# Optimization experiments

Measured on AMD Instinct MI355X. Metric: run time of the kernel, lower is better.

## Reference

```python
import jax, jax.numpy as jnp
import numpy as np

C = 256
H = 8
D = C // H


def setup_inputs() -> dict:
    key = jax.random.key(0)
    ks = jax.random.split(key, 6)
    scale = 1.0 / np.sqrt(C)
    x = jax.random.normal(ks[0], (8, C, 2048), dtype=jnp.float32)
    Wq = jax.random.normal(ks[1], (C, C), dtype=jnp.float32) * scale
    Wk = jax.random.normal(ks[2], (C, C), dtype=jnp.float32) * scale
    Wv = jax.random.normal(ks[3], (C, C), dtype=jnp.float32) * scale
    Wo = jax.random.normal(ks[4], (C, C), dtype=jnp.float32) * scale
    bo = jax.random.normal(ks[5], (C,), dtype=jnp.float32) * 0.01
    return {"x": x, "Wq": Wq, "Wk": Wk, "Wv": Wv, "Wo": Wo, "bo": bo}


def reference(x, Wq, Wk, Wv, Wo, bo):
    # x: [N, C, L]; Conv1d(k=1) == per-position matmul with weight [out, in]
    q = jnp.einsum('oc,ncl->nol', Wq, x)
    k = jnp.einsum('oc,ncl->nol', Wk, x)
    v = jnp.einsum('oc,ncl->nol', Wv, x)
    N, _, L = x.shape
    # rearrange 'n (h d) l -> n l h d'
    q = q.reshape(N, H, D, L).transpose(0, 3, 1, 2)
    k = k.reshape(N, H, D, L).transpose(0, 3, 1, 2)
    v = v.reshape(N, H, D, L).transpose(0, 3, 1, 2)
    qk = jnp.einsum('nqhd,nkhd->nhqk', q, k)
    # NOTE: original scales by full embedding size (channels), not head_dim
    attn = jax.nn.softmax(qk * (C ** -0.5), axis=3)
    out = jnp.einsum('nhql,nlhd->nqhd', attn, v)
    # rearrange 'n l h d -> n (h d) l'
    out = out.transpose(0, 2, 3, 1).reshape(N, C, L)
    return jnp.einsum('oc,ncl->nol', Wo, out) + bo[None, :, None]
```

## Files before the change

kernel.cpp:

```cpp
#include <hip/hip_runtime.h>


typedef __bf16 bf8 __attribute__((ext_vector_type(8)));
typedef float f4 __attribute__((ext_vector_type(4)));
typedef float f32x4 __attribute__((ext_vector_type(4)));
typedef unsigned short u16;
typedef unsigned int u32;
typedef u16 u16x4 __attribute__((ext_vector_type(4)));
typedef u16 u16x8 __attribute__((ext_vector_type(8)));

__device__ __forceinline__ u16 f2bf(float f) {
  __bf16 h = (__bf16)f;
  return __builtin_bit_cast(u16, h);
}
__device__ __forceinline__ float bf2f(u16 b) {
  union { u32 u; float f; } v; v.u = ((u32)b) << 16;
  return v.f;
}
__device__ __forceinline__ u32 pk2bf(float a, float b) {
  return ((u32)f2bf(b) << 16) | (u32)f2bf(a);
}
__device__ __forceinline__ u32 pktrunc(float a, float b) {
  return __builtin_amdgcn_perm(__builtin_bit_cast(u32, b),
                               __builtin_bit_cast(u32, a), 0x07060302u);
}
__device__ __forceinline__ float exp2_fast(float x) {
  return __builtin_amdgcn_exp2f(x);
}

#define MFMA(a, b, c) __builtin_amdgcn_mfma_f32_16x16x32_bf16((a), (b), (c), 0, 0, 0)

union bf8u { u32 u[4]; bf8 v; };
__device__ __forceinline__ bf8 mkbf8(u32 a, u32 b, u32 c, u32 d) {
  bf8u t; t.u[0] = a; t.u[1] = b; t.u[2] = c; t.u[3] = d; return t.v;
}

__global__ __launch_bounds__(256) void convert_weights(
    const float* __restrict__ Wq, const float* __restrict__ Wk,
    const float* __restrict__ Wv, const float* __restrict__ Wo,
    const float* __restrict__ bo,
    u16* __restrict__ Wqb, u16* __restrict__ Wkb, u16* __restrict__ Wvb,
    u16* __restrict__ Wob, u16* __restrict__ bob) {
  const int tid = threadIdx.x;
  const int seg = blockIdx.x >> 6;
  const int blk = blockIdx.x & 63;
  const float* s; u16* d;
  if (seg == 0)      { s = Wq; d = Wqb; }
  else if (seg == 1) { s = Wk; d = Wkb; }
  else if (seg == 2) { s = Wv; d = Wvb; }
  else               { s = Wo; d = Wob; }
  const int base = blk * 1024 + tid * 4;
  f32x4 v = *(const f32x4*)(s + base);
  u16x4 o;
#pragma unroll
  for (int i = 0; i < 4; ++i) o[i] = f2bf(v[i]);
  *(u16x4*)(d + base) = o;
  if (blockIdx.x == 0 && tid < 64) {
    const int bb = tid * 4;
    f32x4 bv = *(const f32x4*)(bo + bb);
    u16x4 ob;
#pragma unroll
    for (int i = 0; i < 4; ++i) ob[i] = f2bf(bv[i]);
    *(u16x4*)(bob + bb) = ob;
  }
}

__global__ __launch_bounds__(256) void qkv_proj(
    const float* __restrict__ x, const u16* __restrict__ Wq,
    const u16* __restrict__ Wk, const u16* __restrict__ Wv,
    u16* __restrict__ qbuf, u16* __restrict__ kbuf, u16* __restrict__ vbuf) {
  __shared__ __align__(16) u16 xt[2][64 * 40];
  const int n = blockIdx.z;
  const int o0 = blockIdx.y * 64;
  const int l0 = blockIdx.x * 64;
  const int tid = threadIdx.x;
  const int w = tid >> 6, lane = tid & 63, quad = lane >> 4, l16 = lane & 15;
  const int ow = o0 + w * 16;
  const float SC = 0.09019327066650391f;

  f4 acc[3][4];
#pragma unroll
  for (int p = 0; p < 3; ++p)
#pragma unroll
    for (int lt = 0; lt < 4; ++lt) acc[p][lt] = (f4){0.f, 0.f, 0.f, 0.f};

  const int cp = tid >> 4;
  const int lq = (tid & 15) * 4;

  auto stage = [&](int c0, int buf) {
    const float* xp = x + (n * 256 + c0 + 2 * cp) * 2048 + l0 + lq;
    f32x4 r0 = *(const f32x4*)xp;
    f32x4 r1 = *(const f32x4*)(xp + 2048);
#pragma unroll
    for (int i = 0; i < 4; ++i)
      *(u32*)&xt[buf][(lq + i) * 40 + 2 * cp] = pk2bf(r0[i], r1[i]);
  };

  stage(0, 0);
  for (int s = 0; s < 8; ++s) {
    __syncthreads();
    if (s < 7) stage((s + 1) * 32, (s + 1) & 1);
    const int c0 = s * 32;
    bf8 a0 = *(const bf8*)(Wq + (ow + l16) * 256 + c0 + quad * 8);
    bf8 a1 = *(const bf8*)(Wk + (ow + l16) * 256 + c0 + quad * 8);
    bf8 a2 = *(const bf8*)(Wv + (ow + l16) * 256 + c0 + quad * 8);
    const u16* xb = xt[s & 1];
#pragma unroll
    for (int lt = 0; lt < 4; ++lt) {
      bf8 b = *(const bf8*)&xb[(lt * 16 + l16) * 40 + quad * 8];
      acc[0][lt] = MFMA(a0, b, acc[0][lt]);
      acc[1][lt] = MFMA(a1, b, acc[1][lt]);
      acc[2][lt] = MFMA(a2, b, acc[2][lt]);
    }
  }
  const int hh = ow >> 5;
  const int dbase = (ow & 31) + quad * 4;
#pragma unroll
  for (int lt = 0; lt < 4; ++lt) {
    const int l = l0 + lt * 16 + l16;
    const int vpos = l0 + (lt >> 1) * 32 + (l16 >> 2) * 8 + (l16 & 3) + (lt & 1) * 4;
    const size_t base = ((size_t)(n * 8 + hh) * 2048 + l) * 32 + dbase;
    u16x4 qv, kv;
#pragma unroll
    for (int r = 0; r < 4; ++r) {
      qv[r] = f2bf(acc[0][lt][r] * SC);
      kv[r] = f2bf(acc[1][lt][r]);
    }
    *(u16x4*)(qbuf + base) = qv;
    *(u16x4*)(kbuf + base) = kv;
#pragma unroll
    for (int r = 0; r < 4; ++r)
      vbuf[(n * 256 + ow + quad * 4 + r) * 2048 + vpos] = f2bf(acc[2][lt][r]);
  }
}

__global__ __launch_bounds__(256) void attn(
    const u16* __restrict__ qbuf, const u16* __restrict__ kbuf,
    const u16* __restrict__ vbuf, u16* __restrict__ abuf) {
  __shared__ float Osh[3][64][37];
  const int head = blockIdx.x, qblk = blockIdx.y;
  const int n = head >> 3, h = head & 7;
  const int tid = threadIdx.x;
  const int w = tid >> 6, lane = tid & 63;
  const int quad = lane >> 4, l16 = lane & 15;
  const int q0 = qblk * 64;
  const int kc0 = w * 512;

  const u16* kb = kbuf + (size_t)head * 2048 * 32 + l16 * 32 + quad * 8;
  const u16* vb = vbuf + ((size_t)n * 256 + h * 32 + l16) * 2048 + quad * 8;

  const bf8 ones = mkbf8(0x3F803F80u, 0x3F803F80u, 0x3F803F80u, 0x3F803F80u);

  bf8 aq[4];
#pragma unroll
  for (int qt = 0; qt < 4; ++qt)
    aq[qt] = *(const bf8*)(qbuf + ((size_t)head * 2048 + q0 + qt * 16 + l16) * 32 + quad * 8);

  f4 O[2][4];
  f4 Lacc[4];
#pragma unroll
  for (int qt = 0; qt < 4; ++qt) {
    O[0][qt] = (f4){0.f, 0.f, 0.f, 0.f};
    O[1][qt] = (f4){0.f, 0.f, 0.f, 0.f};
    Lacc[qt] = (f4){0.f, 0.f, 0.f, 0.f};
  }

  bf8 bk[4], vf[4];
#pragma unroll
  for (int kt = 0; kt < 4; ++kt) bk[kt] = *(const bf8*)(kb + (kc0 + kt * 16) * 32);
#pragma unroll
  for (int dt = 0; dt < 2; ++dt)
#pragma unroll
    for (int g = 0; g < 2; ++g)
      vf[dt * 2 + g] = *(const bf8*)(vb + dt * 16 * 2048 + kc0 + g * 32);

  for (int kc = kc0; kc < kc0 + 512; kc += 64) {
    const int kn = (kc < kc0 + 448) ? kc + 64 : kc0;
    bf8 nk[4], nv[4];
#pragma unroll
    for (int kt = 0; kt < 4; ++kt) nk[kt] = *(const bf8*)(kb + (kn + kt * 16) * 32);
#pragma unroll
    for (int dt = 0; dt < 2; ++dt)
#pragma unroll
      for (int g = 0; g < 2; ++g)
        nv[dt * 2 + g] = *(const bf8*)(vb + dt * 16 * 2048 + kn + g * 32);

#pragma unroll
    for (int qt = 0; qt < 4; ++qt) {
      f4 z = (f4){0.f, 0.f, 0.f, 0.f};
      f4 s0 = MFMA(bk[0], aq[qt], z);
      f4 s1 = MFMA(bk[1], aq[qt], z);
      f4 s2 = MFMA(bk[2], aq[qt], z);
      f4 s3 = MFMA(bk[3], aq[qt], z);
      f4 e0, e1, e2, e3;
#pragma unroll
      for (int r = 0; r < 4; ++r) {
        e0[r] = exp2_fast(s0[r]);
        e1[r] = exp2_fast(s1[r]);
        e2[r] = exp2_fast(s2[r]);
        e3[r] = exp2_fast(s3[r]);
      }
      bf8 B0 = mkbf8(pktrunc(e0[0], e0[1]), pktrunc(e0[2], e0[3]),
                     pktrunc(e1[0], e1[1]), pktrunc(e1[2], e1[3]));
      bf8 B1 = mkbf8(pktrunc(e2[0], e2[1]), pktrunc(e2[2], e2[3]),
                     pktrunc(e3[0], e3[1]), pktrunc(e3[2], e3[3]));
      Lacc[qt] = MFMA(ones, B0, Lacc[qt]);
      Lacc[qt] = MFMA(ones, B1, Lacc[qt]);
#pragma unroll
      for (int dt = 0; dt < 2; ++dt) {
        f4 o = O[dt][qt];
        o = MFMA(vf[dt * 2 + 0], B0, o);
        o = MFMA(vf[dt * 2 + 1], B1, o);
        O[dt][qt] = o;
      }
    }
#pragma unroll
    for (int i = 0; i < 4; ++i) { bk[i] = nk[i]; vf[i] = nv[i]; }
  }

  if (w > 0) {
#pragma unroll
    for (int dt = 0; dt < 2; ++dt)
#pragma unroll
      for (int qt = 0; qt < 4; ++qt)
#pragma unroll
        for (int r = 0; r < 4; ++r)
          Osh[w - 1][lane][dt * 16 + qt * 4 + r] = O[dt][qt][r];
#pragma unroll
    for (int qt = 0; qt < 4; ++qt)
      Osh[w - 1][lane][32 + qt] = Lacc[qt][0];
  }
  __syncthreads();
  if (w == 0) {
#pragma unroll
    for (int p = 0; p < 3; ++p) {
#pragma unroll
      for (int dt = 0; dt < 2; ++dt)
#pragma unroll
        for (int qt = 0; qt < 4; ++qt)
#pragma unroll
          for (int r = 0; r < 4; ++r)
            O[dt][qt][r] += Osh[p][lane][dt * 16 + qt * 4 + r];
#pragma unroll
      for (int qt = 0; qt < 4; ++qt)
        Lacc[qt][0] += Osh[p][lane][32 + qt];
    }
#pragma unroll
    for (int qt = 0; qt < 4; ++qt) {
      const float inv = 1.0f / Lacc[qt][0];
      const int q = q0 + qt * 16 + l16;
#pragma unroll
      for (int dt = 0; dt < 2; ++dt) {
        u16x4 ov;
#pragma unroll
        for (int r = 0; r < 4; ++r) ov[r] = f2bf(O[dt][qt][r] * inv);
        *(u16x4*)(abuf + ((size_t)n * 2048 + q) * 256 + h * 32 + dt * 16 + quad * 4) = ov;
      }
    }
  }
}

__global__ __launch_bounds__(256) void out_proj(
    const u16* __restrict__ abuf, const u16* __restrict__ Wo,
    const u16* __restrict__ bo, float* __restrict__ out) {
  const int n = blockIdx.z;
  const int o0 = blockIdx.y * 64;
  const int l0 = blockIdx.x * 64;
  const int tid = threadIdx.x;
  const int w = tid >> 6, lane = tid & 63, quad = lane >> 4, l16 = lane & 15;
  const int ow = o0 + w * 16;

  const u16* wp = Wo + (ow + l16) * 256 + quad * 8;
  const u16* ab = abuf + ((size_t)n * 2048 + l0 + l16) * 256 + quad * 8;

  f4 acc[4];
#pragma unroll
  for (int lt = 0; lt < 4; ++lt) acc[lt] = (f4){0.f, 0.f, 0.f, 0.f};

  bf8 a = *(const bf8*)wp;
  bf8 b[4];
#pragma unroll
  for (int lt = 0; lt < 4; ++lt) b[lt] = *(const bf8*)(ab + lt * 16 * 256);

  for (int c0 = 0; c0 < 256; c0 += 32) {
    const int cn = (c0 < 224) ? c0 + 32 : 0;
    bf8 na = *(const bf8*)(wp + cn);
    bf8 nb[4];
#pragma unroll
    for (int lt = 0; lt < 4; ++lt)
      nb[lt] = *(const bf8*)(ab + lt * 16 * 256 + cn);
#pragma unroll
    for (int lt = 0; lt < 4; ++lt) acc[lt] = MFMA(a, b[lt], acc[lt]);
    a = na;
#pragma unroll
    for (int lt = 0; lt < 4; ++lt) b[lt] = nb[lt];
  }
#pragma unroll
  for (int r = 0; r < 4; ++r) {
    const int o = ow + quad * 4 + r;
    const float bias = bf2f(bo[o]);
#pragma unroll
    for (int lt = 0; lt < 4; ++lt) {
      out[((size_t)n * 256 + o) * 2048 + l0 + lt * 16 + l16] = acc[lt][r] + bias;
    }
  }
}

extern "C" void kernel_launch(void* const* d_in, const int* in_sizes, int n_in,
                              void* d_out, int out_size, void* d_ws, size_t ws_size,
                              hipStream_t stream) {
  const float* x  = (const float*)d_in[0];
  const float* Wq = (const float*)d_in[1];
  const float* Wk = (const float*)d_in[2];
  const float* Wv = (const float*)d_in[3];
  const float* Wo = (const float*)d_in[4];
  const float* bo = (const float*)d_in[5];
  float* out = (float*)d_out;

  u16* ws = (u16*)d_ws;
  u16* qbuf = ws;
  u16* kbuf = qbuf + 4194304;
  u16* vbuf = kbuf + 4194304;
  u16* abuf = vbuf + 4194304;
  u16* Wqb  = abuf + 4194304;
  u16* Wkb  = Wqb + 65536;
  u16* Wvb  = Wkb + 65536;
  u16* Wob  = Wvb + 65536;
  u16* bob  = Wob + 65536;

  convert_weights<<<dim3(256), 256, 0, stream>>>(Wq, Wk, Wv, Wo, bo,
                                                 Wqb, Wkb, Wvb, Wob, bob);
  qkv_proj<<<dim3(32, 4, 8), 256, 0, stream>>>(x, Wqb, Wkb, Wvb,
                                               qbuf, kbuf, vbuf);
  attn<<<dim3(64, 32), 256, 0, stream>>>(qbuf, kbuf, vbuf, abuf);
  out_proj<<<dim3(32, 4, 8), 256, 0, stream>>>(abuf, Wob, bob, out);
}
```

Measured before the change: 173.3 us.

## Fold weight conversion into projections, stage full x tile, vectorize V stores

Removes the separate convert_weights launch: the fp32 weights and bias are now read directly and packed to bf16 in registers inside qkv_proj and out_proj. qkv_proj stages the whole 64x256 x tile into shared memory once, replacing the double-buffered per-step staging and its repeated barriers. The V product is computed with swapped MFMA operands so that it can be written as 8-wide vector stores. The cost is more global fp32 weight traffic and extra conversion work per block, plus a larger shared-memory footprint that may reduce occupancy.

```diff
diff --git a/kernel.cpp b/kernel.cpp
--- a/kernel.cpp
+++ b/kernel.cpp
@@ -13,10 +13,6 @@
   __bf16 h = (__bf16)f;
   return __builtin_bit_cast(u16, h);
 }
-__device__ __forceinline__ float bf2f(u16 b) {
-  union { u32 u; float f; } v; v.u = ((u32)b) << 16;
-  return v.f;
-}
 __device__ __forceinline__ u32 pk2bf(float a, float b) {
   return ((u32)f2bf(b) << 16) | (u32)f2bf(a);
 }
@@ -34,42 +30,18 @@
 __device__ __forceinline__ bf8 mkbf8(u32 a, u32 b, u32 c, u32 d) {
   bf8u t; t.u[0] = a; t.u[1] = b; t.u[2] = c; t.u[3] = d; return t.v;
 }
-
-__global__ __launch_bounds__(256) void convert_weights(
-    const float* __restrict__ Wq, const float* __restrict__ Wk,
-    const float* __restrict__ Wv, const float* __restrict__ Wo,
-    const float* __restrict__ bo,
-    u16* __restrict__ Wqb, u16* __restrict__ Wkb, u16* __restrict__ Wvb,
-    u16* __restrict__ Wob, u16* __restrict__ bob) {
-  const int tid = threadIdx.x;
-  const int seg = blockIdx.x >> 6;
-  const int blk = blockIdx.x & 63;
-  const float* s; u16* d;
-  if (seg == 0)      { s = Wq; d = Wqb; }
-  else if (seg == 1) { s = Wk; d = Wkb; }
-  else if (seg == 2) { s = Wv; d = Wvb; }
-  else               { s = Wo; d = Wob; }
-  const int base = blk * 1024 + tid * 4;
-  f32x4 v = *(const f32x4*)(s + base);
-  u16x4 o;
-#pragma unroll
-  for (int i = 0; i < 4; ++i) o[i] = f2bf(v[i]);
-  *(u16x4*)(d + base) = o;
-  if (blockIdx.x == 0 && tid < 64) {
-    const int bb = tid * 4;
-    f32x4 bv = *(const f32x4*)(bo + bb);
-    u16x4 ob;
-#pragma unroll
-    for (int i = 0; i < 4; ++i) ob[i] = f2bf(bv[i]);
-    *(u16x4*)(bob + bb) = ob;
-  }
+__device__ __forceinline__ bf8 ldw8(const float* p) {
+  f32x4 u = *(const f32x4*)p;
+  f32x4 v = *(const f32x4*)(p + 4);
+  return mkbf8(pk2bf(u[0], u[1]), pk2bf(u[2], u[3]),
+               pk2bf(v[0], v[1]), pk2bf(v[2], v[3]));
 }
 
 __global__ __launch_bounds__(256) void qkv_proj(
-    const float* __restrict__ x, const u16* __restrict__ Wq,
-    const u16* __restrict__ Wk, const u16* __restrict__ Wv,
+    const float* __restrict__ x, const float* __restrict__ Wq,
+    const float* __restrict__ Wk, const float* __restrict__ Wv,
     u16* __restrict__ qbuf, u16* __restrict__ kbuf, u16* __restrict__ vbuf) {
-  __shared__ __align__(16) u16 xt[2][64 * 40];
+  __shared__ __align__(16) u16 xt[64 * 264];
   const int n = blockIdx.z;
   const int o0 = blockIdx.y * 64;
   const int l0 = blockIdx.x * 64;
@@ -78,59 +50,70 @@
   const int ow = o0 + w * 16;
   const float SC = 0.09019327066650391f;
 
-  f4 acc[3][4];
-#pragma unroll
-  for (int p = 0; p < 3; ++p)
-#pragma unroll
-    for (int lt = 0; lt < 4; ++lt) acc[p][lt] = (f4){0.f, 0.f, 0.f, 0.f};
-
-  const int cp = tid >> 4;
+  const int cp2 = tid >> 4;
   const int lq = (tid & 15) * 4;
-
-  auto stage = [&](int c0, int buf) {
-    const float* xp = x + (n * 256 + c0 + 2 * cp) * 2048 + l0 + lq;
+#pragma unroll
+  for (int it = 0; it < 8; ++it) {
+    const float* xp = x + (size_t)(n * 256 + it * 32 + 2 * cp2) * 2048 + l0 + lq;
     f32x4 r0 = *(const f32x4*)xp;
     f32x4 r1 = *(const f32x4*)(xp + 2048);
 #pragma unroll
     for (int i = 0; i < 4; ++i)
-      *(u32*)&xt[buf][(lq + i) * 40 + 2 * cp] = pk2bf(r0[i], r1[i]);
-  };
-
-  stage(0, 0);
+      *(u32*)&xt[(lq + i) * 264 + it * 32 + 2 * cp2] = pk2bf(r0[i], r1[i]);
+  }
+  __syncthreads();
+
+  f4 accq[4], acck[4], accv[4];
+#pragma unroll
+  for (int lt = 0; lt < 4; ++lt) {
+    accq[lt] = (f4){0.f, 0.f, 0.f, 0.f};
+    acck[lt] = (f4){0.f, 0.f, 0.f, 0.f};
+    accv[lt] = (f4){0.f, 0.f, 0.f, 0.f};
+  }
+
+  const float* wqp = Wq + (ow + l16) * 256 + quad * 8;
+  const float* wkp = Wk + (ow + l16) * 256 + quad * 8;
+  const float* wvp = Wv + (ow + l16) * 256 + quad * 8;
+
+#pragma unroll
   for (int s = 0; s < 8; ++s) {
-    __syncthreads();
-    if (s < 7) stage((s + 1) * 32, (s + 1) & 1);
     const int c0 = s * 32;
-    bf8 a0 = *(const bf8*)(Wq + (ow + l16) * 256 + c0 + quad * 8);
-    bf8 a1 = *(const bf8*)(Wk + (ow + l16) * 256 + c0 + quad * 8);
-    bf8 a2 = *(const bf8*)(Wv + (ow + l16) * 256 + c0 + quad * 8);
-    const u16* xb = xt[s & 1];
+    bf8 a0 = ldw8(wqp + c0);
+    bf8 a1 = ldw8(wkp + c0);
+    bf8 a2 = ldw8(wvp + c0);
 #pragma unroll
     for (int lt = 0; lt < 4; ++lt) {
-      bf8 b = *(const bf8*)&xb[(lt * 16 + l16) * 40 + quad * 8];
-      acc[0][lt] = MFMA(a0, b, acc[0][lt]);
-      acc[1][lt] = MFMA(a1, b, acc[1][lt]);
-      acc[2][lt] = MFMA(a2, b, acc[2][lt]);
-    }
-  }
+      bf8 b = *(const bf8*)&xt[(lt * 16 + l16) * 264 + c0 + quad * 8];
+      accq[lt] = MFMA(a0, b, accq[lt]);
+      acck[lt] = MFMA(a1, b, acck[lt]);
+      accv[lt] = MFMA(b, a2, accv[lt]);
+    }
+  }
+
   const int hh = ow >> 5;
   const int dbase = (ow & 31) + quad * 4;
 #pragma unroll
   for (int lt = 0; lt < 4; ++lt) {
     const int l = l0 + lt * 16 + l16;
-    const int vpos = l0 + (lt >> 1) * 32 + (l16 >> 2) * 8 + (l16 & 3) + (lt & 1) * 4;
     const size_t base = ((size_t)(n * 8 + hh) * 2048 + l) * 32 + dbase;
     u16x4 qv, kv;
 #pragma unroll
     for (int r = 0; r < 4; ++r) {
-      qv[r] = f2bf(acc[0][lt][r] * SC);
-      kv[r] = f2bf(acc[1][lt][r]);
+      qv[r] = f2bf(accq[lt][r] * SC);
+      kv[r] = f2bf(acck[lt][r]);
     }
     *(u16x4*)(qbuf + base) = qv;
     *(u16x4*)(kbuf + base) = kv;
-#pragma unroll
-    for (int r = 0; r < 4; ++r)
-      vbuf[(n * 256 + ow + quad * 4 + r) * 2048 + vpos] = f2bf(acc[2][lt][r]);
+  }
+#pragma unroll
+  for (int g = 0; g < 2; ++g) {
+    u16x8 vv;
+#pragma unroll
+    for (int r = 0; r < 4; ++r) {
+      vv[r] = f2bf(accv[2 * g][r]);
+      vv[4 + r] = f2bf(accv[2 * g + 1][r]);
+    }
+    *(u16x8*)(vbuf + ((size_t)(n * 256 + ow + l16)) * 2048 + l0 + g * 32 + quad * 8) = vv;
   }
 }
 
@@ -261,8 +244,8 @@
 }
 
 __global__ __launch_bounds__(256) void out_proj(
-    const u16* __restrict__ abuf, const u16* __restrict__ Wo,
-    const u16* __restrict__ bo, float* __restrict__ out) {
+    const u16* __restrict__ abuf, const float* __restrict__ Wo,
+    const float* __restrict__ bo, float* __restrict__ out) {
   const int n = blockIdx.z;
   const int o0 = blockIdx.y * 64;
   const int l0 = blockIdx.x * 64;
@@ -270,35 +253,37 @@
   const int w = tid >> 6, lane = tid & 63, quad = lane >> 4, l16 = lane & 15;
   const int ow = o0 + w * 16;
 
-  const u16* wp = Wo + (ow + l16) * 256 + quad * 8;
+  const float* wp = Wo + (ow + l16) * 256 + quad * 8;
   const u16* ab = abuf + ((size_t)n * 2048 + l0 + l16) * 256 + quad * 8;
 
   f4 acc[4];
 #pragma unroll
   for (int lt = 0; lt < 4; ++lt) acc[lt] = (f4){0.f, 0.f, 0.f, 0.f};
 
-  bf8 a = *(const bf8*)wp;
+  f32x4 wa0 = *(const f32x4*)wp, wa1 = *(const f32x4*)(wp + 4);
   bf8 b[4];
 #pragma unroll
   for (int lt = 0; lt < 4; ++lt) b[lt] = *(const bf8*)(ab + lt * 16 * 256);
 
   for (int c0 = 0; c0 < 256; c0 += 32) {
     const int cn = (c0 < 224) ? c0 + 32 : 0;
-    bf8 na = *(const bf8*)(wp + cn);
+    f32x4 wn0 = *(const f32x4*)(wp + cn), wn1 = *(const f32x4*)(wp + cn + 4);
     bf8 nb[4];
 #pragma unroll
     for (int lt = 0; lt < 4; ++lt)
       nb[lt] = *(const bf8*)(ab + lt * 16 * 256 + cn);
+    bf8 a = mkbf8(pk2bf(wa0[0], wa0[1]), pk2bf(wa0[2], wa0[3]),
+                  pk2bf(wa1[0], wa1[1]), pk2bf(wa1[2], wa1[3]));
 #pragma unroll
     for (int lt = 0; lt < 4; ++lt) acc[lt] = MFMA(a, b[lt], acc[lt]);
-    a = na;
+    wa0 = wn0; wa1 = wn1;
 #pragma unroll
     for (int lt = 0; lt < 4; ++lt) b[lt] = nb[lt];
   }
 #pragma unroll
   for (int r = 0; r < 4; ++r) {
     const int o = ow + quad * 4 + r;
-    const float bias = bf2f(bo[o]);
+    const float bias = bo[o];
 #pragma unroll
     for (int lt = 0; lt < 4; ++lt) {
       out[((size_t)n * 256 + o) * 2048 + l0 + lt * 16 + l16] = acc[lt][r] + bias;
@@ -322,16 +307,9 @@
   u16* kbuf = qbuf + 4194304;
   u16* vbuf = kbuf + 4194304;
   u16* abuf = vbuf + 4194304;
-  u16* Wqb  = abuf + 4194304;
-  u16* Wkb  = Wqb + 65536;
-  u16* Wvb  = Wkb + 65536;
-  u16* Wob  = Wvb + 65536;
-  u16* bob  = Wob + 65536;
-
-  convert_weights<<<dim3(256), 256, 0, stream>>>(Wq, Wk, Wv, Wo, bo,
-                                                 Wqb, Wkb, Wvb, Wob, bob);
-  qkv_proj<<<dim3(32, 4, 8), 256, 0, stream>>>(x, Wqb, Wkb, Wvb,
+
+  qkv_proj<<<dim3(32, 4, 8), 256, 0, stream>>>(x, Wq, Wk, Wv,
                                                qbuf, kbuf, vbuf);
   attn<<<dim3(64, 32), 256, 0, stream>>>(qbuf, kbuf, vbuf, abuf);
-  out_proj<<<dim3(32, 4, 8), 256, 0, stream>>>(abuf, Wob, bob, out);
-}
+  out_proj<<<dim3(32, 4, 8), 256, 0, stream>>>(abuf, Wo, bo, out);
+}
```

After: 183.8 us. +6.0%, slower.

## Compute softmax row sums with VALU adds and vectorize V stores

Applied to the files above, without the earlier changes.

In the attention kernel, the ones-matrix MFMAs that accumulated the softmax denominator are replaced by per-lane float adds of the fp32 exponentials, followed by a cross-quad shuffle reduction. The explicit register double-buffering of K/V loads is removed, leaving prefetch to the compiler. In the QKV projection, V is computed with swapped MFMA operands so each lane holds contiguous positions, letting V be written with 16-byte vector stores instead of scattered 2-byte stores. This frees MFMA issue slots and store bandwidth, at the cost of extra VALU work and possibly less latency hiding for K/V loads.

```diff
diff --git a/kernel.cpp b/kernel.cpp
--- a/kernel.cpp
+++ b/kernel.cpp
@@ -78,11 +78,13 @@
   const int ow = o0 + w * 16;
   const float SC = 0.09019327066650391f;
 
-  f4 acc[3][4];
-#pragma unroll
-  for (int p = 0; p < 3; ++p)
-#pragma unroll
-    for (int lt = 0; lt < 4; ++lt) acc[p][lt] = (f4){0.f, 0.f, 0.f, 0.f};
+  f4 accq[4], acck[4], accv[4];
+#pragma unroll
+  for (int lt = 0; lt < 4; ++lt) {
+    accq[lt] = (f4){0.f, 0.f, 0.f, 0.f};
+    acck[lt] = (f4){0.f, 0.f, 0.f, 0.f};
+    accv[lt] = (f4){0.f, 0.f, 0.f, 0.f};
+  }
 
   const int cp = tid >> 4;
   const int lq = (tid & 15) * 4;
@@ -108,29 +110,36 @@
 #pragma unroll
     for (int lt = 0; lt < 4; ++lt) {
       bf8 b = *(const bf8*)&xb[(lt * 16 + l16) * 40 + quad * 8];
-      acc[0][lt] = MFMA(a0, b, acc[0][lt]);
-      acc[1][lt] = MFMA(a1, b, acc[1][lt]);
-      acc[2][lt] = MFMA(a2, b, acc[2][lt]);
-    }
-  }
+      accq[lt] = MFMA(a0, b, accq[lt]);
+      acck[lt] = MFMA(a1, b, acck[lt]);
+      accv[lt] = MFMA(b, a2, accv[lt]);
+    }
+  }
+
   const int hh = ow >> 5;
   const int dbase = (ow & 31) + quad * 4;
 #pragma unroll
   for (int lt = 0; lt < 4; ++lt) {
     const int l = l0 + lt * 16 + l16;
-    const int vpos = l0 + (lt >> 1) * 32 + (l16 >> 2) * 8 + (l16 & 3) + (lt & 1) * 4;
     const size_t base = ((size_t)(n * 8 + hh) * 2048 + l) * 32 + dbase;
     u16x4 qv, kv;
 #pragma unroll
     for (int r = 0; r < 4; ++r) {
-      qv[r] = f2bf(acc[0][lt][r] * SC);
-      kv[r] = f2bf(acc[1][lt][r]);
+      qv[r] = f2bf(accq[lt][r] * SC);
+      kv[r] = f2bf(acck[lt][r]);
     }
     *(u16x4*)(qbuf + base) = qv;
     *(u16x4*)(kbuf + base) = kv;
-#pragma unroll
-    for (int r = 0; r < 4; ++r)
-      vbuf[(n * 256 + ow + quad * 4 + r) * 2048 + vpos] = f2bf(acc[2][lt][r]);
+  }
+#pragma unroll
+  for (int g = 0; g < 2; ++g) {
+    u16x8 vv;
+#pragma unroll
+    for (int r = 0; r < 4; ++r) {
+      vv[r] = f2bf(accv[2 * g][r]);
+      vv[4 + r] = f2bf(accv[2 * g + 1][r]);
+    }
+    *(u16x8*)(vbuf + ((size_t)(n * 256 + ow + l16)) * 2048 + l0 + g * 32 + quad * 8) = vv;
   }
 }
 
@@ -149,41 +158,29 @@
   const u16* kb = kbuf + (size_t)head * 2048 * 32 + l16 * 32 + quad * 8;
   const u16* vb = vbuf + ((size_t)n * 256 + h * 32 + l16) * 2048 + quad * 8;
 
-  const bf8 ones = mkbf8(0x3F803F80u, 0x3F803F80u, 0x3F803F80u, 0x3F803F80u);
-
   bf8 aq[4];
 #pragma unroll
   for (int qt = 0; qt < 4; ++qt)
     aq[qt] = *(const bf8*)(qbuf + ((size_t)head * 2048 + q0 + qt * 16 + l16) * 32 + quad * 8);
 
   f4 O[2][4];
-  f4 Lacc[4];
+  float lsum[4];
 #pragma unroll
   for (int qt = 0; qt < 4; ++qt) {
     O[0][qt] = (f4){0.f, 0.f, 0.f, 0.f};
     O[1][qt] = (f4){0.f, 0.f, 0.f, 0.f};
-    Lacc[qt] = (f4){0.f, 0.f, 0.f, 0.f};
-  }
-
-  bf8 bk[4], vf[4];
-#pragma unroll
-  for (int kt = 0; kt < 4; ++kt) bk[kt] = *(const bf8*)(kb + (kc0 + kt * 16) * 32);
-#pragma unroll
-  for (int dt = 0; dt < 2; ++dt)
-#pragma unroll
-    for (int g = 0; g < 2; ++g)
-      vf[dt * 2 + g] = *(const bf8*)(vb + dt * 16 * 2048 + kc0 + g * 32);
+    lsum[qt] = 0.f;
+  }
 
   for (int kc = kc0; kc < kc0 + 512; kc += 64) {
-    const int kn = (kc < kc0 + 448) ? kc + 64 : kc0;
-    bf8 nk[4], nv[4];
-#pragma unroll
-    for (int kt = 0; kt < 4; ++kt) nk[kt] = *(const bf8*)(kb + (kn + kt * 16) * 32);
+    bf8 bk[4], vf[4];
+#pragma unroll
+    for (int kt = 0; kt < 4; ++kt) bk[kt] = *(const bf8*)(kb + (kc + kt * 16) * 32);
 #pragma unroll
     for (int dt = 0; dt < 2; ++dt)
 #pragma unroll
       for (int g = 0; g < 2; ++g)
-        nv[dt * 2 + g] = *(const bf8*)(vb + dt * 16 * 2048 + kn + g * 32);
+        vf[dt * 2 + g] = *(const bf8*)(vb + dt * 16 * 2048 + kc + g * 32);
 
 #pragma unroll
     for (int qt = 0; qt < 4; ++qt) {
@@ -200,12 +197,13 @@
         e2[r] = exp2_fast(s2[r]);
         e3[r] = exp2_fast(s3[r]);
       }
+      f4 t01 = e0 + e1, t23 = e2 + e3;
+      f4 t = t01 + t23;
+      lsum[qt] += (t[0] + t[1]) + (t[2] + t[3]);
       bf8 B0 = mkbf8(pktrunc(e0[0], e0[1]), pktrunc(e0[2], e0[3]),
                      pktrunc(e1[0], e1[1]), pktrunc(e1[2], e1[3]));
       bf8 B1 = mkbf8(pktrunc(e2[0], e2[1]), pktrunc(e2[2], e2[3]),
                      pktrunc(e3[0], e3[1]), pktrunc(e3[2], e3[3]));
-      Lacc[qt] = MFMA(ones, B0, Lacc[qt]);
-      Lacc[qt] = MFMA(ones, B1, Lacc[qt]);
 #pragma unroll
       for (int dt = 0; dt < 2; ++dt) {
         f4 o = O[dt][qt];
@@ -214,8 +212,14 @@
         O[dt][qt] = o;
       }
     }
-#pragma unroll
-    for (int i = 0; i < 4; ++i) { bk[i] = nk[i]; vf[i] = nv[i]; }
+  }
+
+#pragma unroll
+  for (int qt = 0; qt < 4; ++qt) {
+    float s = lsum[qt];
+    s += __shfl_xor(s, 16);
+    s += __shfl_xor(s, 32);
+    lsum[qt] = s;
   }
 
   if (w > 0) {
@@ -228,7 +232,7 @@
           Osh[w - 1][lane][dt * 16 + qt * 4 + r] = O[dt][qt][r];
 #pragma unroll
     for (int qt = 0; qt < 4; ++qt)
-      Osh[w - 1][lane][32 + qt] = Lacc[qt][0];
+      Osh[w - 1][lane][32 + qt] = lsum[qt];
   }
   __syncthreads();
   if (w == 0) {
@@ -243,11 +247,11 @@
             O[dt][qt][r] += Osh[p][lane][dt * 16 + qt * 4 + r];
 #pragma unroll
       for (int qt = 0; qt < 4; ++qt)
-        Lacc[qt][0] += Osh[p][lane][32 + qt];
+        lsum[qt] += Osh[p][lane][32 + qt];
     }
 #pragma unroll
     for (int qt = 0; qt < 4; ++qt) {
-      const float inv = 1.0f / Lacc[qt][0];
+      const float inv = 1.0f / lsum[qt];
       const int q = q0 + qt * 16 + l16;
 #pragma unroll
       for (int dt = 0; dt < 2; ++dt) {
```

New measurement: 165.6 us, median of 2. -4.4%, faster.
